# Kernel optimization log

Measured on AMD Instinct MI355X. Metric: run time of the kernel, lower is better.

## Reference

```python
import jax, jax.numpy as jnp
import numpy as np

B, S, T = 32, 512, 512           # batch, text len, decoder steps
ENC, ATT = 512, 128              # encoder_dim, attention_dim
PH, PO = 256, 256                # prenet hidden/output
DEC, M = 1024, 128               # decoder_rnn_dim, num_mels


def setup_inputs() -> dict:
    key = jax.random.key(0)
    ks = jax.random.split(key, 16)

    def w(k, shape, fan_in):
        return jax.random.normal(k, shape, jnp.float32) / np.float32(np.sqrt(fan_in))

    return {
        "encoder_outputs": jax.random.normal(ks[0], (B, S, ENC), jnp.float32),
        "target_mels": jax.random.normal(ks[1], (B, T, M), jnp.float32),
        # PreNet (dropout in eval mode => identity)
        "pn_w1": w(ks[2], (M, PH), M), "pn_b1": jnp.zeros((PH,), jnp.float32),
        "pn_w2": w(ks[3], (PH, PO), PH), "pn_b2": jnp.zeros((PO,), jnp.float32),
        # AdditiveAttention
        "att_we": w(ks[4], (ENC, ATT), ENC), "att_be": jnp.zeros((ATT,), jnp.float32),
        "att_wd": w(ks[5], (DEC, ATT), DEC), "att_bd": jnp.zeros((ATT,), jnp.float32),
        "att_v": w(ks[6], (ATT,), ATT), "att_vb": jnp.zeros((), jnp.float32),
        # GRU (PyTorch layout: W_ih [3H, in], W_hh [3H, H], gate order r,z,n)
        "gru_wih": w(ks[7], (3 * DEC, PO + ENC), PO + ENC),
        "gru_whh": w(ks[8], (3 * DEC, DEC), DEC),
        "gru_bih": jnp.zeros((3 * DEC,), jnp.float32),
        "gru_bhh": jnp.zeros((3 * DEC,), jnp.float32),
        # output / stop projections
        "out_w": w(ks[9], (DEC + ENC, M), DEC + ENC), "out_b": jnp.zeros((M,), jnp.float32),
        "stop_w": w(ks[10], (DEC + ENC, 1), DEC + ENC), "stop_b": jnp.zeros((1,), jnp.float32),
    }


def reference(encoder_outputs, target_mels, pn_w1, pn_b1, pn_w2, pn_b2,
              att_we, att_be, att_wd, att_bd, att_v, att_vb,
              gru_wih, gru_whh, gru_bih, gru_bhh,
              out_w, out_b, stop_w, stop_b):
    b, t, m = target_mels.shape
    # encoder projection is time-invariant: hoist out of the step loop
    enc_proj = encoder_outputs @ att_we + att_be              # [B,S,A]

    # teacher forcing: prev_mel at step 0 is zeros, then target_mels[:, t-1]
    prev_mels = jnp.concatenate(
        [jnp.zeros((1, b, m), target_mels.dtype),
         jnp.transpose(target_mels, (1, 0, 2))[:-1]], axis=0)  # [T,B,M]

    h0 = jnp.zeros((b, gru_whh.shape[1]), encoder_outputs.dtype)  # [B,DEC]

    def step(h, prev_mel):
        # PreNet (eval mode: dropout = identity)
        x = jax.nn.relu(prev_mel @ pn_w1 + pn_b1)
        x = jax.nn.relu(x @ pn_w2 + pn_b2)                     # [B,PO]
        # additive attention
        dproj = h @ att_wd + att_bd                            # [B,A]
        scores = jnp.tanh(enc_proj + dproj[:, None, :]) @ att_v + att_vb  # [B,S]
        aw = jax.nn.softmax(scores, axis=1)                    # [B,S]
        context = jnp.einsum('bs,bse->be', aw, encoder_outputs)  # [B,ENC]
        # GRU cell (PyTorch gate math, order r,z,n)
        rin = jnp.concatenate([x, context], axis=-1)           # [B,PO+ENC]
        gi = rin @ gru_wih.T + gru_bih                         # [B,3*DEC]
        gh = h @ gru_whh.T + gru_bhh
        ir, iz, inn = jnp.split(gi, 3, axis=-1)
        hr, hz, hn = jnp.split(gh, 3, axis=-1)
        r = jax.nn.sigmoid(ir + hr)
        z = jax.nn.sigmoid(iz + hz)
        n = jnp.tanh(inn + r * hn)
        h_new = (1.0 - z) * n + z * h                          # [B,DEC]
        # projections
        dout = jnp.concatenate([h_new, context], axis=-1)      # [B,DEC+ENC]
        mel = dout @ out_w + out_b                             # [B,M]
        stop = (dout @ stop_w + stop_b)[:, 0]                  # [B]
        return h_new, (mel, stop, aw)

    _, (mels, stops, aws) = jax.lax.scan(step, h0, prev_mels)
    mel_outputs = jnp.transpose(mels, (1, 0, 2))               # [B,T,M]
    stop_tokens = stops.T                                      # [B,T]
    attention_weights = jnp.transpose(aws, (1, 0, 2))          # [B,T,S]
    return (mel_outputs, stop_tokens, attention_weights)
```

## Files before the change

### kernel.cpp

```cpp
#include <hip/hip_runtime.h>

constexpr int B_   = 32;
constexpr int S_   = 512;
constexpr int T_   = 512;
constexpr int ENC_ = 512;
constexpr int ATT_ = 128;
constexpr int PO_  = 256;
constexpr int DEC_ = 1024;
constexpr int M_   = 128;

constexpr int MEL_OFF  = 0;
constexpr int STOP_OFF = B_*T_*M_;
constexpr int AW_OFF   = STOP_OFF + B_*T_;

typedef __attribute__((ext_vector_type(8))) short bf16x8;
typedef __attribute__((ext_vector_type(4))) float f32x4;
typedef unsigned long long ull;

__device__ __forceinline__ float frcp(float x){ return __builtin_amdgcn_rcpf(x); }
__device__ __forceinline__ float ftanh(float x){ float e = __expf(2.f*x); return 1.f - 2.f*frcp(e + 1.f); }
__device__ __forceinline__ float fsig(float x){ return frcp(1.f + __expf(-x)); }

__device__ __forceinline__ float2 upk2(unsigned u){
    return make_float2(__builtin_bit_cast(float, u << 16),
                       __builtin_bit_cast(float, u & 0xffff0000u));
}
__device__ __forceinline__ unsigned short f2b(float f){
    unsigned u = __builtin_bit_cast(unsigned, f);
    return (unsigned short)((u + 0x7fffu + ((u >> 16) & 1u)) >> 16);
}
__device__ __forceinline__ unsigned pk2(float a, float b){
    return (unsigned)f2b(a) | ((unsigned)f2b(b) << 16);
}

__device__ __forceinline__ float ald(const float* p){
    return __hip_atomic_load(p, __ATOMIC_RELAXED, __HIP_MEMORY_SCOPE_AGENT);
}
__device__ __forceinline__ ull ald64(const void* p){
    return __hip_atomic_load((const ull*)p, __ATOMIC_RELAXED, __HIP_MEMORY_SCOPE_AGENT);
}
__device__ __forceinline__ unsigned aldu(const unsigned* p){
    return __hip_atomic_load(p, __ATOMIC_RELAXED, __HIP_MEMORY_SCOPE_AGENT);
}
__device__ __forceinline__ void astf(float* p, float v){
    __hip_atomic_store(p, v, __ATOMIC_RELAXED, __HIP_MEMORY_SCOPE_AGENT);
}
union F2U { float2 f; ull u; };
__device__ __forceinline__ void ast2f(float* p, float a, float b){
    F2U x; x.f = make_float2(a, b);
    __hip_atomic_store((ull*)p, x.u, __ATOMIC_RELAXED, __HIP_MEMORY_SCOPE_AGENT);
}
__device__ __forceinline__ void astu(unsigned* p, unsigned v){
    __hip_atomic_store(p, v, __ATOMIC_RELAXED, __HIP_MEMORY_SCOPE_AGENT);
}

__device__ __forceinline__ void waitP64(const unsigned* f, unsigned ep){
    if (threadIdx.x < 64){
        for (;;){
            unsigned v = aldu(&f[threadIdx.x*16]);
            if (__all(v >= ep)) break;
            __builtin_amdgcn_s_sleep(1);
        }
    }
    __syncthreads();
}
__device__ __forceinline__ void waitP128(const unsigned* f, unsigned ep){
    if (threadIdx.x < 64){
        for (;;){
            unsigned a = aldu(&f[threadIdx.x*16]);
            unsigned b = aldu(&f[(threadIdx.x + 64)*16]);
            unsigned m = a < b ? a : b;
            if (__all(m >= ep)) break;
            __builtin_amdgcn_s_sleep(1);
        }
    }
    __syncthreads();
}
__device__ __forceinline__ void signalF(unsigned* f, unsigned v){
    asm volatile("s_waitcnt vmcnt(0) lgkmcnt(0)" ::: "memory");
    __syncthreads();
    if (threadIdx.x == 0) astu(f, v);
}

__device__ __forceinline__ f32x4 mfma16(bf16x8 a, bf16x8 b, f32x4 c){
    return __builtin_amdgcn_mfma_f32_16x16x32_bf16(a, b, c, 0, 0, 0);
}

__global__ __launch_bounds__(256) void k_prep_w(const float* __restrict__ enc,
        const float* __restrict__ whh, const float* __restrict__ wih,
        const float* __restrict__ oww,
        unsigned short* __restrict__ enc_b, unsigned short* __restrict__ wgh,
        unsigned short* __restrict__ wgx, unsigned short* __restrict__ wgc,
        unsigned short* __restrict__ ow_b){
    long long idx = (long long)blockIdx.x*256 + threadIdx.x;
    if (idx < 8388608LL){
        int bh = (int)(idx >> 17); int r = (int)(idx & 131071);
        int s = r >> 9, e = r & 511;
        int b = bh >> 1, half = bh & 1;
        enc_b[idx] = f2b(enc[((size_t)b*S_ + half*256 + s)*ENC_ + e]);
    } else if (idx < 11534336LL){
        long long q = idx - 8388608LL;
        int ds = (int)(q / 98304); int r = (int)(q % 98304);
        int jc = r / 16384; int r2 = r % 16384;
        int kc = r2 >> 9, l = (r2 >> 3) & 63, e = r2 & 7;
        int j = (jc >> 1)*1024 + ds*32 + (jc & 1)*16 + (l & 15);
        int k = kc*32 + ((l >> 4) << 3) + e;
        wgh[q] = f2b(whh[(size_t)j*DEC_ + k]);
    } else if (idx < 12320768LL){
        long long q = idx - 11534336LL;
        int ds = (int)(q / 24576); int r = (int)(q % 24576);
        int jc = r / 4096; int r3 = r % 4096;
        int kc = r3 >> 9, l = (r3 >> 3) & 63, e = r3 & 7;
        int j = (jc >> 1)*1024 + ds*32 + (jc & 1)*16 + (l & 15);
        int k = kc*32 + ((l >> 4) << 3) + e;
        wgx[q] = f2b(wih[(size_t)j*768 + k]);
    } else if (idx < 13893632LL){
        long long q = idx - 12320768LL;
        int ds = (int)(q / 49152); int r = (int)(q % 49152);
        int jc = r / 8192; int r3 = r % 8192;
        int kc = r3 >> 9, l = (r3 >> 3) & 63, e = r3 & 7;
        int j = (jc >> 1)*1024 + ds*32 + (jc & 1)*16 + (l & 15);
        int k = kc*32 + ((l >> 4) << 3) + e;
        wgc[q] = f2b(wih[(size_t)j*768 + 256 + k]);
    } else if (idx < 14090240LL){
        long long q = idx - 13893632LL;
        int cg = (int)(q / 49152); int r = (int)(q % 49152);
        int oc = r / 1536, k = r % 1536;
        ow_b[q] = f2b(oww[(size_t)k*M_ + cg*32 + oc]);
    }
}

__global__ __launch_bounds__(256) void k_encproj(const float* __restrict__ enc,
        const float* __restrict__ we, const float* __restrict__ be,
        unsigned short* __restrict__ ep_b){
    __shared__ float we_s[64*128];
    __shared__ float enc_s[64*64];
    int blk = blockIdx.x, tid = threadIdx.x;
    int b = blk >> 3, ss = blk & 7;
    int s = tid >> 2, ag = tid & 3;
    float acc[32];
    #pragma unroll
    for (int j = 0; j < 32; ++j) acc[j] = 0.f;
    for (int kc = 0; kc < 8; ++kc){
        __syncthreads();
        for (int i = tid; i < 8192; i += 256)
            we_s[i] = we[(size_t)(kc*64 + (i >> 7))*ATT_ + (i & 127)];
        for (int i = tid; i < 4096; i += 256)
            enc_s[i] = enc[((size_t)b*S_ + ss*64 + (i >> 6))*ENC_ + kc*64 + (i & 63)];
        __syncthreads();
        for (int kk = 0; kk < 64; ++kk){
            float ev = enc_s[s*64 + kk];
            const float* wr = &we_s[(kk << 7) + (ag << 5)];
            #pragma unroll
            for (int j = 0; j < 32; ++j) acc[j] += ev*wr[j];
        }
    }
    #pragma unroll
    for (int j = 0; j < 32; ++j){
        int a = (ag << 5) + j;
        ep_b[((size_t)b*512 + ss*64 + s)*ATT_ + a] = f2b(acc[j] + be[a]);
    }
}

__global__ __launch_bounds__(128) void k_prenet(const float* __restrict__ tm,
        const float* __restrict__ w1, const float* __restrict__ b1,
        const float* __restrict__ w2, const float* __restrict__ b2,
        unsigned short* __restrict__ xall){
    __shared__ float mel_l[128*20];
    __shared__ float h1_l[256*20];
    int row0 = blockIdx.x << 4;
    int t = row0 >> 5, b0 = row0 & 31;
    int tid = threadIdx.x;
    for (int p = 0; p < 16; p++){
        int idx = tid + (p << 7);
        int k = idx & 127, r = idx >> 7;
        float v = 0.f;
        if (t > 0) v = tm[((size_t)(b0 + r)*T_ + (t - 1))*M_ + k];
        mel_l[k*20 + r] = v;
    }
    __syncthreads();
    float acc1[16], acc2[16];
    #pragma unroll
    for (int i = 0; i < 16; i++){ acc1[i] = 0.f; acc2[i] = 0.f; }
    for (int k = 0; k < M_; k++){
        float wa = w1[k*256 + tid];
        float wb = w1[k*256 + tid + 128];
        float mv[16];
        *(float4*)&mv[0]  = *(const float4*)&mel_l[k*20 + 0];
        *(float4*)&mv[4]  = *(const float4*)&mel_l[k*20 + 4];
        *(float4*)&mv[8]  = *(const float4*)&mel_l[k*20 + 8];
        *(float4*)&mv[12] = *(const float4*)&mel_l[k*20 + 12];
        #pragma unroll
        for (int r = 0; r < 16; r++){ acc1[r] += mv[r]*wa; acc2[r] += mv[r]*wb; }
    }
    float bb1a = b1[tid], bb1b = b1[tid + 128];
    #pragma unroll
    for (int r = 0; r < 16; r++){
        h1_l[tid*20 + r]         = fmaxf(acc1[r] + bb1a, 0.f);
        h1_l[(tid + 128)*20 + r] = fmaxf(acc2[r] + bb1b, 0.f);
    }
    __syncthreads();
    #pragma unroll
    for (int i = 0; i < 16; i++){ acc1[i] = 0.f; acc2[i] = 0.f; }
    for (int k = 0; k < 256; k++){
        float wa = w2[k*256 + tid];
        float wb = w2[k*256 + tid + 128];
        float mv[16];
        *(float4*)&mv[0]  = *(const float4*)&h1_l[k*20 + 0];
        *(float4*)&mv[4]  = *(const float4*)&h1_l[k*20 + 4];
        *(float4*)&mv[8]  = *(const float4*)&h1_l[k*20 + 8];
        *(float4*)&mv[12] = *(const float4*)&h1_l[k*20 + 12];
        #pragma unroll
        for (int r = 0; r < 16; r++){ acc1[r] += mv[r]*wa; acc2[r] += mv[r]*wb; }
    }
    float bb2a = b2[tid], bb2b = b2[tid + 128];
    #pragma unroll
    for (int r = 0; r < 16; r++){
        xall[((size_t)row0 + r)*PO_ + tid]       = f2b(fmaxf(acc1[r] + bb2a, 0.f));
        xall[((size_t)row0 + r)*PO_ + tid + 128] = f2b(fmaxf(acc2[r] + bb2b, 0.f));
    }
}

#define DYN_BYTES 110592

struct KP {
    const unsigned short* xall_b; const unsigned short* enc_b; const unsigned short* ep_b;
    const unsigned short* wgh; const unsigned short* wgx; const unsigned short* wgc;
    const unsigned short* ow_b;
    const float* awd; const float* sw; const float* bd; const float* av; const float* avb;
    const float* bih; const float* bhh; const float* p_ob; const float* p_sb;
    float* h_f32; unsigned short* h_fb;
    unsigned short* ctx_b; float* den; float* es_b; float* dpp;
    unsigned* gflag; unsigned* aflag; unsigned* mflag; float* out;
};

__global__ __launch_bounds__(1024) void k_persist(KP p){
    extern __shared__ char sm[];
    const int bid = blockIdx.x, tid = threadIdx.x;
    const int lane = tid & 63;

    if (bid < 64){
        const int xcd = bid & 7, slot8 = bid >> 3;
        const int ds = xcd*4 + (slot8 >> 1), bh = slot8 & 1;
        unsigned short* hf_b = (unsigned short*)sm;
        char* cf = sm;
        float* pgh_l = (float*)(sm + 32768);
        float* pgx_l = (float*)(sm + 45568);
        float* pgc_l = (float*)(sm + 58368);
        float* h_l   = (float*)(sm + 71168);
        float* rden_l= (float*)(sm + 73216);
        float h_reg = 0.f;

        for (int t = 0; t < T_; ++t){
            waitP64(p.gflag, (unsigned)t);
            {
                const ull* shb = (const ull*)p.h_fb + (size_t)(t & 1)*8192;
                for (int i = tid; i < 4096; i += 1024){
                    int u = i & 1, l = (i >> 1) & 63, kc = i >> 7;
                    ((ull*)hf_b)[i] = ald64(&shb[(((size_t)bh*32 + kc)*64 + l)*2 + u]);
                }
                __syncthreads();
                int w = tid >> 6;
                if (w < 12){
                    int jc = w >> 1, kg = w & 1;
                    int r4 = lane >> 4, c16 = lane & 15;
                    const bf16x8* Bh = (const bf16x8*)p.wgh +
                        ((size_t)(ds*6 + jc)*32)*64 + lane;
                    f32x4 acc = {0.f,0.f,0.f,0.f};
                    #pragma unroll
                    for (int c = 0; c < 16; ++c){
                        int kc = kg*16 + c;
                        bf16x8 a = *(const bf16x8*)(hf_b + ((kc*64 + lane) << 3));
                        acc = mfma16(a, Bh[kc*64], acc);
                    }
                    #pragma unroll
                    for (int r = 0; r < 4; ++r)
                        pgh_l[(kg*16 + r4*4 + r)*100 + jc*16 + c16] = acc[r];
                    const bf16x8* Xp = (const bf16x8*)p.wgx +
                        ((size_t)(ds*6 + jc)*8)*64 + lane;
                    f32x4 ax = {0.f,0.f,0.f,0.f};
                    #pragma unroll
                    for (int c = 0; c < 4; ++c){
                        int kc = kg*4 + c;
                        bf16x8 a = *(const bf16x8*)(p.xall_b +
                            ((size_t)t*32 + bh*16 + c16)*256 + kc*32 + r4*8);
                        ax = mfma16(a, Xp[kc*64], ax);
                    }
                    #pragma unroll
                    for (int r = 0; r < 4; ++r)
                        pgx_l[(kg*16 + r4*4 + r)*100 + jc*16 + c16] = ax[r];
                }
                __syncthreads();
            }
            waitP64(p.aflag, (unsigned)(t + 1));
            {
                const int slot = t & 3;
                if (tid < 16){
                    int b = bh*16 + tid;
                    rden_l[tid] = frcp(ald(&p.den[slot*64 + b]) +
                                       ald(&p.den[slot*64 + 32 + b]));
                }
                __syncthreads();
                {
                    int i = tid;
                    int kc = i >> 6, l = i & 63;
                    int b = bh*16 + (l & 15);
                    int e0 = kc*32 + ((l >> 4) << 3);
                    const ull* c0 = (const ull*)p.ctx_b + (((size_t)slot*2 + 0)*32 + b)*128 + (e0 >> 2);
                    const ull* c1 = (const ull*)p.ctx_b + (((size_t)slot*2 + 1)*32 + b)*128 + (e0 >> 2);
                    ull u00 = ald64(c0), u01 = ald64(c0 + 1);
                    ull u10 = ald64(c1), u11 = ald64(c1 + 1);
                    float rd = rden_l[l & 15];
                    uint2 x0 = __builtin_bit_cast(uint2, u00);
                    uint2 x1 = __builtin_bit_cast(uint2, u01);
                    uint2 y0 = __builtin_bit_cast(uint2, u10);
                    uint2 y1 = __builtin_bit_cast(uint2, u11);
                    float2 a0 = upk2(x0.x), b0 = upk2(y0.x);
                    float2 a1 = upk2(x0.y), b1 = upk2(y0.y);
                    float2 a2 = upk2(x1.x), b2 = upk2(y1.x);
                    float2 a3 = upk2(x1.y), b3 = upk2(y1.y);
                    unsigned w0 = pk2((a0.x + b0.x)*rd, (a0.y + b0.y)*rd);
                    unsigned w1 = pk2((a1.x + b1.x)*rd, (a1.y + b1.y)*rd);
                    unsigned w2 = pk2((a2.x + b2.x)*rd, (a2.y + b2.y)*rd);
                    unsigned w3 = pk2((a3.x + b3.x)*rd, (a3.y + b3.y)*rd);
                    *(uint4*)(cf + (size_t)i*16) = make_uint4(w0, w1, w2, w3);
                }
                __syncthreads();
                int w = tid >> 6;
                if (w < 12){
                    int jc = w >> 1, kg = w & 1;
                    int r4 = lane >> 4, c16 = lane & 15;
                    const bf16x8* Cp = (const bf16x8*)p.wgc +
                        ((size_t)(ds*6 + jc)*16)*64 + lane;
                    f32x4 acc = {0.f,0.f,0.f,0.f};
                    #pragma unroll
                    for (int c = 0; c < 8; ++c){
                        int kc = kg*8 + c;
                        bf16x8 a = *(const bf16x8*)(cf + ((kc*64 + lane) << 4));
                        acc = mfma16(a, Cp[kc*64], acc);
                    }
                    #pragma unroll
                    for (int r = 0; r < 4; ++r)
                        pgc_l[(kg*16 + r4*4 + r)*100 + jc*16 + c16] = acc[r];
                }
                __syncthreads();
                if (tid < 512){
                    int b16 = tid >> 5, dl = tid & 31;
                    int dglob = ds*32 + dl;
                    const float* pa = pgh_l + b16*100;
                    const float* pb = pgh_l + (16 + b16)*100;
                    const float* xa = pgx_l + b16*100;
                    const float* xb = pgx_l + (16 + b16)*100;
                    const float* ca = pgc_l + b16*100;
                    const float* cb = pgc_l + (16 + b16)*100;
                    float gi_r = xa[dl]      + xb[dl]      + ca[dl]      + cb[dl]      + p.bih[dglob];
                    float gi_z = xa[32 + dl] + xb[32 + dl] + ca[32 + dl] + cb[32 + dl] + p.bih[1024 + dglob];
                    float gi_n = xa[64 + dl] + xb[64 + dl] + ca[64 + dl] + cb[64 + dl] + p.bih[2048 + dglob];
                    float gh_r = pa[dl]      + pb[dl]      + p.bhh[dglob];
                    float gh_z = pa[32 + dl] + pb[32 + dl] + p.bhh[1024 + dglob];
                    float gh_n = pa[64 + dl] + pb[64 + dl] + p.bhh[2048 + dglob];
                    float rr = fsig(gi_r + gh_r);
                    float zz = fsig(gi_z + gh_z);
                    float nn = ftanh(gi_n + rr*gh_n);
                    float hv = (1.f - zz)*nn + zz*h_reg;
                    h_reg = hv;
                    h_l[b16*32 + dl] = hv;
                    float hv1 = __shfl_xor(hv, 1);
                    if (!(dl & 1)){
                        int b = bh*16 + b16;
                        ast2f(&p.h_f32[(size_t)((t + 1) & 3)*32768 + (size_t)b*1024 + dglob], hv, hv1);
                        unsigned pkv = pk2(hv, hv1);
                        int l2 = ((dl >> 3) << 4) + b16;
                        size_t fo = (size_t)((t + 1) & 1)*16384 +
                                    (((size_t)bh*32 + ds)*64 + l2)*4 + ((dl & 7) >> 1);
                        astu((unsigned*)p.h_fb + fo, pkv);
                    }
                }
                __syncthreads();
                {
                    int b16 = tid >> 6, ag = tid & 63;
                    int a0 = ag*2;
                    const float* ar = p.awd + (size_t)(ds*32)*128 + a0;
                    float s0 = 0.f, s1 = 0.f;
                    #pragma unroll 8
                    for (int dl = 0; dl < 32; ++dl){
                        float hd = h_l[b16*32 + dl];
                        float2 w2 = *(const float2*)(ar + (size_t)dl*128);
                        s0 += hd*w2.x; s1 += hd*w2.y;
                    }
                    ast2f(&p.dpp[(((size_t)ds*2 + bh)*16 + b16)*128 + a0], s0, s1);
                }
            }
            signalF(&p.gflag[bid*16], (unsigned)(t + 1));
        }
    } else if (bid < 128){
        const int aa = bid - 64, b = aa >> 1, half = aa & 1;
        unsigned short* ep_l = (unsigned short*)sm;
        float* red  = (float*)(sm + 67584);
        float* sred = (float*)(sm + 100992);
        float* dpl  = (float*)(sm + 105088);
        float* avl  = (float*)(sm + 105600);
        float* esl  = (float*)(sm + 106112);
        float* eslt = (float*)(sm + 107136);
        {
            const ull* src = (const ull*)(p.ep_b + ((size_t)b*512 + half*256)*128);
            for (int i = tid; i < 8192; i += 1024){
                int row = i >> 5, col = i & 31;
                ((ull*)ep_l)[(size_t)row*33 + col] = src[i];
            }
            if (tid < 128) avl[tid] = p.av[tid];
        }
        __syncthreads();
        for (int t = 0; t < T_; ++t){
            waitP64(p.gflag, (unsigned)t);
            if (t >= 3) waitP128(p.mflag, (unsigned)(t - 2));
            const int slot = t & 3;
            {
                int a = tid & 127, g = tid >> 7;
                const int bhb = b >> 4, b15 = b & 15;
                float s = 0.f;
                #pragma unroll
                for (int i = 0; i < 4; ++i){
                    int ds2 = g*4 + i;
                    s += ald(&p.dpp[(((size_t)ds2*2 + bhb)*16 + b15)*128 + a]);
                }
                red[g*128 + a] = s;
            }
            __syncthreads();
            if (tid < 128){
                float s = p.bd[tid];
                #pragma unroll
                for (int g = 0; g < 8; ++g) s += red[g*128 + tid];
                dpl[tid] = s;
            }
            __syncthreads();
            {
                int s = tid >> 2, ao = tid & 3;
                const ull* er = (const ull*)ep_l + (size_t)s*33 + ao*8;
                float sc = 0.f;
                #pragma unroll
                for (int i = 0; i < 8; ++i){
                    uint2 uu = __builtin_bit_cast(uint2, er[i]);
                    float2 e0 = upk2(uu.x), e1 = upk2(uu.y);
                    int a0 = ao*32 + i*4;
                    sc += ftanh(e0.x + dpl[a0])*avl[a0]
                        + ftanh(e0.y + dpl[a0+1])*avl[a0+1]
                        + ftanh(e1.x + dpl[a0+2])*avl[a0+2]
                        + ftanh(e1.y + dpl[a0+3])*avl[a0+3];
                }
                sred[tid] = sc;
            }
            __syncthreads();
            if (tid < 256){
                float sc = sred[tid*4] + sred[tid*4+1] + sred[tid*4+2] + sred[tid*4+3] + p.avb[0];
                float ev = __expf(sc);
                esl[tid] = ev;
                eslt[(tid & 15)*17 + (tid >> 4)] = ev;
                astf(&p.es_b[(size_t)slot*16384 + b*512 + half*256 + tid], ev);
            }
            __syncthreads();
            if (tid < 64){
                float d = esl[tid*4] + esl[tid*4+1] + esl[tid*4+2] + esl[tid*4+3];
                #pragma unroll
                for (int m = 1; m <= 32; m <<= 1) d += __shfl_xor(d, m);
                if (tid == 0) astf(&p.den[slot*64 + half*32 + b], d);
            }
            {
                int eo = tid >> 4, sg = tid & 15;
                int e8 = eo*8;
                const unsigned short* eb = p.enc_b + ((size_t)b*2 + half)*131072;
                float a0=0,a1=0,a2=0,a3=0,a4=0,a5=0,a6=0,a7=0;
                #pragma unroll 4
                for (int i = 0; i < 16; ++i){
                    int s = sg*16 + i;
                    float ev = eslt[i*17 + sg];
                    uint4 u = *(const uint4*)(eb + (size_t)s*512 + e8);
                    float2 v0=upk2(u.x), v1=upk2(u.y), v2=upk2(u.z), v3=upk2(u.w);
                    a0+=ev*v0.x; a1+=ev*v0.y; a2+=ev*v1.x; a3+=ev*v1.y;
                    a4+=ev*v2.x; a5+=ev*v2.y; a6+=ev*v3.x; a7+=ev*v3.y;
                }
                float* rr = &red[sg*522 + e8];
                rr[0]=a0; rr[1]=a1; rr[2]=a2; rr[3]=a3;
                rr[4]=a4; rr[5]=a5; rr[6]=a6; rr[7]=a7;
            }
            __syncthreads();
            if (tid < 512){
                float c = 0.f;
                #pragma unroll
                for (int sg = 0; sg < 16; ++sg) c += red[sg*522 + tid];
                float c1 = __shfl_xor(c, 1);
                if (!(tid & 1))
                    astu((unsigned*)p.ctx_b + (((size_t)slot*2 + half)*32 + b)*256 + (tid >> 1),
                         pk2(c, c1));
            }
            signalF(&p.aflag[aa*16], (unsigned)(t + 1));
        }
    } else {
        const int m = bid - 128, b = m >> 2, q = m & 3;
        unsigned short* ow_l = (unsigned short*)sm;
        float* dout = (float*)(sm + 98432);
        float* redm = (float*)(sm + 104576);
        float* rdm  = (float*)(sm + 108800);
        float* stpr = (float*)(sm + 108816);
        {
            const ull* src = (const ull*)p.ow_b + (size_t)q*12288;
            for (int i = tid; i < 12288; i += 1024){
                int oc = i / 384, kq = i - oc*384;
                uint2 u = __builtin_bit_cast(uint2, src[i]);
                unsigned* d = (unsigned*)ow_l + (size_t)oc*769 + kq*2;
                d[0] = u.x; d[1] = u.y;
            }
        }
        __syncthreads();
        for (int t = 1; t <= T_; ++t){
            waitP64(p.gflag, (unsigned)t);
            waitP64(p.aflag, (unsigned)t);
            const int slot = (t - 1) & 3;
            if (tid < 512){
                ull u = ald64((const ull*)p.h_f32 + (size_t)(t & 3)*16384 + (size_t)b*512 + tid);
                *(float2*)&dout[tid*2] = __builtin_bit_cast(float2, u);
            } else if (tid < 768){
                int i = tid - 512;
                unsigned u0 = aldu((const unsigned*)p.ctx_b + (((size_t)slot*2 + 0)*32 + b)*256 + i);
                unsigned u1 = aldu((const unsigned*)p.ctx_b + (((size_t)slot*2 + 1)*32 + b)*256 + i);
                float2 f0 = upk2(u0), f1 = upk2(u1);
                *(float2*)&dout[1024 + i*2] = make_float2(f0.x + f1.x, f0.y + f1.y);
            } else if (tid == 1023){
                rdm[0] = frcp(ald(&p.den[slot*64 + b]) + ald(&p.den[slot*64 + 32 + b]));
            }
            __syncthreads();
            if (tid < 512) dout[1024 + tid] *= rdm[0];
            __syncthreads();
            {
                int kg = tid >> 5, oc = tid & 31;
                const unsigned* wr = (const unsigned*)ow_l + (size_t)oc*769 + kg*24;
                const float* dr = dout + kg*48;
                float a = 0.f;
                #pragma unroll 6
                for (int i = 0; i < 24; ++i){
                    float2 w2 = upk2(wr[i]);
                    a += dr[i*2]*w2.x + dr[i*2+1]*w2.y;
                }
                redm[kg*33 + oc] = a;
            }
            if (q == 0 && tid < 512){
                int k3 = tid*3;
                float s = dout[k3]*p.sw[k3] + dout[k3+1]*p.sw[k3+1] + dout[k3+2]*p.sw[k3+2];
                #pragma unroll
                for (int mm = 1; mm <= 32; mm <<= 1) s += __shfl_xor(s, mm);
                if ((tid & 63) == 0) stpr[tid >> 6] = s;
                float ev = ald(&p.es_b[(size_t)slot*16384 + b*512 + tid]);
                p.out[AW_OFF + ((size_t)b*T_ + (t-1))*S_ + tid] = ev*rdm[0];
            }
            __syncthreads();
            if (tid < 32){
                float a = 0.f;
                #pragma unroll
                for (int kg = 0; kg < 32; ++kg) a += redm[kg*33 + tid];
                int c = q*32 + tid;
                p.out[MEL_OFF + ((size_t)b*T_ + (t-1))*M_ + c] = a + p.p_ob[c];
            } else if (tid == 32 && q == 0){
                float tot = 0.f;
                #pragma unroll
                for (int w2 = 0; w2 < 8; ++w2) tot += stpr[w2];
                p.out[STOP_OFF + (size_t)b*T_ + (t-1)] = tot + p.p_sb[0];
            }
            signalF(&p.mflag[m*16], (unsigned)t);
        }
    }
}

extern "C" void kernel_launch(void* const* d_in, const int* in_sizes, int n_in,
                              void* d_out, int out_size, void* d_ws, size_t ws_size,
                              hipStream_t stream){
    const float* enc = (const float*)d_in[0];
    const float* tm  = (const float*)d_in[1];
    const float* pw1 = (const float*)d_in[2];
    const float* pb1 = (const float*)d_in[3];
    const float* pw2 = (const float*)d_in[4];
    const float* pb2 = (const float*)d_in[5];
    const float* awe = (const float*)d_in[6];
    const float* abe = (const float*)d_in[7];
    const float* awd = (const float*)d_in[8];
    const float* abd = (const float*)d_in[9];
    const float* av  = (const float*)d_in[10];
    const float* avb = (const float*)d_in[11];
    const float* wih = (const float*)d_in[12];
    const float* whh = (const float*)d_in[13];
    const float* bih = (const float*)d_in[14];
    const float* bhh = (const float*)d_in[15];
    const float* oww = (const float*)d_in[16];
    const float* obb = (const float*)d_in[17];
    const float* sww = (const float*)d_in[18];
    const float* sbb = (const float*)d_in[19];
    float* out = (float*)d_out;
    float* ws  = (float*)d_ws;

    unsigned short* xall_b = (unsigned short*)ws;
    unsigned short* enc_b  = (unsigned short*)(ws + 2097152);
    unsigned short* ep_b   = (unsigned short*)(ws + 6291456);
    unsigned short* wgh    = (unsigned short*)(ws + 7340032);
    unsigned short* wgx    = (unsigned short*)(ws + 8912896);
    unsigned short* wgc    = (unsigned short*)(ws + 9306112);
    unsigned short* ow_b   = (unsigned short*)(ws + 10092544);
    float* h_f32 = ws + 10190848;
    unsigned short* h_fb   = (unsigned short*)(ws + 10321920);
    unsigned short* ctx_b  = (unsigned short*)(ws + 10354688);
    float* den  = ws + 10420224;
    float* es_b = ws + 10420480;
    float* dpp  = ws + 10486016;
    unsigned* gflag = (unsigned*)(ws + 10617088);
    unsigned* aflag = gflag + 1024;
    unsigned* mflag = aflag + 1024;

    hipMemsetAsync(h_f32, 0, (size_t)131072*4, stream);
    hipMemsetAsync(h_fb, 0, (size_t)65536*2, stream);
    hipMemsetAsync(dpp, 0, (size_t)131072*4, stream);
    hipMemsetAsync(gflag, 0, 16384, stream);

    k_prep_w<<<55040, 256, 0, stream>>>(enc, whh, wih, oww,
                                        enc_b, wgh, wgx, wgc, ow_b);
    k_encproj<<<256, 256, 0, stream>>>(enc, awe, abe, ep_b);
    k_prenet<<<1024, 128, 0, stream>>>(tm, pw1, pb1, pw2, pb2, xall_b);

    hipFuncSetAttribute((const void*)k_persist,
                        hipFuncAttributeMaxDynamicSharedMemorySize, DYN_BYTES);

    KP kp;
    kp.xall_b = xall_b; kp.enc_b = enc_b; kp.ep_b = ep_b;
    kp.wgh = wgh; kp.wgx = wgx; kp.wgc = wgc; kp.ow_b = ow_b;
    kp.awd = awd; kp.sw = sww; kp.bd = abd; kp.av = av; kp.avb = avb;
    kp.bih = bih; kp.bhh = bhh; kp.p_ob = obb; kp.p_sb = sbb;
    kp.h_f32 = h_f32; kp.h_fb = h_fb;
    kp.ctx_b = ctx_b; kp.den = den; kp.es_b = es_b; kp.dpp = dpp;
    kp.gflag = gflag; kp.aflag = aflag; kp.mflag = mflag; kp.out = out;

    KP* kparg = &kp;
    void* args[] = { (void*)kparg };
    hipLaunchCooperativeKernel((void*)k_persist, dim3(256), dim3(1024),
                               args, DYN_BYTES, stream);
}
```

Before: 15.28 ms.

## Move decoder-state attention projection from GRU blocks into attention blocks

GRU blocks no longer compute partial h·W_d products into a global dpp buffer. Each attention block now loads the full fp32 hidden state for its batch row and computes the 128-wide projection itself against a transposed fp32 copy of att_wd made in the prep kernel. This removes a __syncthreads and a matvec from the GRU critical path and drops the dpp scratch buffer. The cost is a 1024-long dot product per attention block each step, duplicated across the two halves. Flag stride also shrinks from 16 to 4 words and the spin sleep doubles, which changes polling cache-line sharing and latency.

```diff
diff --git a/kernel.cpp b/kernel.cpp
--- a/kernel.cpp
+++ b/kernel.cpp
@@ -57,9 +57,9 @@
 __device__ __forceinline__ void waitP64(const unsigned* f, unsigned ep){
     if (threadIdx.x < 64){
         for (;;){
-            unsigned v = aldu(&f[threadIdx.x*16]);
+            unsigned v = aldu(&f[threadIdx.x*4]);
             if (__all(v >= ep)) break;
-            __builtin_amdgcn_s_sleep(1);
+            __builtin_amdgcn_s_sleep(2);
         }
     }
     __syncthreads();
@@ -67,11 +67,11 @@
 __device__ __forceinline__ void waitP128(const unsigned* f, unsigned ep){
     if (threadIdx.x < 64){
         for (;;){
-            unsigned a = aldu(&f[threadIdx.x*16]);
-            unsigned b = aldu(&f[(threadIdx.x + 64)*16]);
+            unsigned a = aldu(&f[threadIdx.x*4]);
+            unsigned b = aldu(&f[(threadIdx.x + 64)*4]);
             unsigned m = a < b ? a : b;
             if (__all(m >= ep)) break;
-            __builtin_amdgcn_s_sleep(1);
+            __builtin_amdgcn_s_sleep(2);
         }
     }
     __syncthreads();
@@ -88,10 +88,10 @@
 
 __global__ __launch_bounds__(256) void k_prep_w(const float* __restrict__ enc,
         const float* __restrict__ whh, const float* __restrict__ wih,
-        const float* __restrict__ oww,
+        const float* __restrict__ awd, const float* __restrict__ oww,
         unsigned short* __restrict__ enc_b, unsigned short* __restrict__ wgh,
         unsigned short* __restrict__ wgx, unsigned short* __restrict__ wgc,
-        unsigned short* __restrict__ ow_b){
+        unsigned short* __restrict__ ow_b, float* __restrict__ wdT32){
     long long idx = (long long)blockIdx.x*256 + threadIdx.x;
     if (idx < 8388608LL){
         int bh = (int)(idx >> 17); int r = (int)(idx & 131071);
@@ -127,6 +127,10 @@
         int cg = (int)(q / 49152); int r = (int)(q % 49152);
         int oc = r / 1536, k = r % 1536;
         ow_b[q] = f2b(oww[(size_t)k*M_ + cg*32 + oc]);
+    } else if (idx < 14221312LL){
+        long long q = idx - 14090240LL;
+        int a = (int)(q >> 10), k = (int)(q & 1023);
+        wdT32[q] = awd[(size_t)k*M_ + a];
     }
 }
 
@@ -227,10 +231,10 @@
     const unsigned short* xall_b; const unsigned short* enc_b; const unsigned short* ep_b;
     const unsigned short* wgh; const unsigned short* wgx; const unsigned short* wgc;
     const unsigned short* ow_b;
-    const float* awd; const float* sw; const float* bd; const float* av; const float* avb;
+    const float* wdT32; const float* sw; const float* bd; const float* av; const float* avb;
     const float* bih; const float* bhh; const float* p_ob; const float* p_sb;
     float* h_f32; unsigned short* h_fb;
-    unsigned short* ctx_b; float* den; float* es_b; float* dpp;
+    unsigned short* ctx_b; float* den; float* es_b;
     unsigned* gflag; unsigned* aflag; unsigned* mflag; float* out;
 };
 
@@ -247,7 +251,6 @@
         float* pgh_l = (float*)(sm + 32768);
         float* pgx_l = (float*)(sm + 45568);
         float* pgc_l = (float*)(sm + 58368);
-        float* h_l   = (float*)(sm + 71168);
         float* rden_l= (float*)(sm + 73216);
         float h_reg = 0.f;
 
@@ -364,7 +367,6 @@
                     float nn = ftanh(gi_n + rr*gh_n);
                     float hv = (1.f - zz)*nn + zz*h_reg;
                     h_reg = hv;
-                    h_l[b16*32 + dl] = hv;
                     float hv1 = __shfl_xor(hv, 1);
                     if (!(dl & 1)){
                         int b = bh*16 + b16;
@@ -376,28 +378,15 @@
                         astu((unsigned*)p.h_fb + fo, pkv);
                     }
                 }
-                __syncthreads();
-                {
-                    int b16 = tid >> 6, ag = tid & 63;
-                    int a0 = ag*2;
-                    const float* ar = p.awd + (size_t)(ds*32)*128 + a0;
-                    float s0 = 0.f, s1 = 0.f;
-                    #pragma unroll 8
-                    for (int dl = 0; dl < 32; ++dl){
-                        float hd = h_l[b16*32 + dl];
-                        float2 w2 = *(const float2*)(ar + (size_t)dl*128);
-                        s0 += hd*w2.x; s1 += hd*w2.y;
-                    }
-                    ast2f(&p.dpp[(((size_t)ds*2 + bh)*16 + b16)*128 + a0], s0, s1);
-                }
-            }
-            signalF(&p.gflag[bid*16], (unsigned)(t + 1));
+            }
+            signalF(&p.gflag[bid*4], (unsigned)(t + 1));
         }
     } else if (bid < 128){
         const int aa = bid - 64, b = aa >> 1, half = aa & 1;
         unsigned short* ep_l = (unsigned short*)sm;
         float* red  = (float*)(sm + 67584);
         float* sred = (float*)(sm + 100992);
+        float* h_lf = (float*)(sm + 100992);
         float* dpl  = (float*)(sm + 105088);
         float* avl  = (float*)(sm + 105600);
         float* esl  = (float*)(sm + 106112);
@@ -415,16 +404,22 @@
             waitP64(p.gflag, (unsigned)t);
             if (t >= 3) waitP128(p.mflag, (unsigned)(t - 2));
             const int slot = t & 3;
+            if (tid < 512)
+                ((ull*)h_lf)[tid] = ald64((const ull*)p.h_f32 +
+                    (size_t)(t & 3)*16384 + (size_t)b*512 + tid);
+            __syncthreads();
             {
-                int a = tid & 127, g = tid >> 7;
-                const int bhb = b >> 4, b15 = b & 15;
+                int a = tid & 127, kg = tid >> 7;
+                const float* hw = h_lf + kg*128;
+                const float* wr = p.wdT32 + (size_t)a*1024 + kg*128;
                 float s = 0.f;
-                #pragma unroll
-                for (int i = 0; i < 4; ++i){
-                    int ds2 = g*4 + i;
-                    s += ald(&p.dpp[(((size_t)ds2*2 + bhb)*16 + b15)*128 + a]);
-                }
-                red[g*128 + a] = s;
+                #pragma unroll 8
+                for (int i = 0; i < 128; i += 4){
+                    float4 h4 = *(const float4*)(hw + i);
+                    float4 w4 = *(const float4*)(wr + i);
+                    s += h4.x*w4.x + h4.y*w4.y + h4.z*w4.z + h4.w*w4.w;
+                }
+                red[kg*128 + a] = s;
             }
             __syncthreads();
             if (tid < 128){
@@ -493,7 +488,7 @@
                     astu((unsigned*)p.ctx_b + (((size_t)slot*2 + half)*32 + b)*256 + (tid >> 1),
                          pk2(c, c1));
             }
-            signalF(&p.aflag[aa*16], (unsigned)(t + 1));
+            signalF(&p.aflag[aa*4], (unsigned)(t + 1));
         }
     } else {
         const int m = bid - 128, b = m >> 2, q = m & 3;
@@ -565,7 +560,7 @@
                 for (int w2 = 0; w2 < 8; ++w2) tot += stpr[w2];
                 p.out[STOP_OFF + (size_t)b*T_ + (t-1)] = tot + p.p_sb[0];
             }
-            signalF(&p.mflag[m*16], (unsigned)t);
+            signalF(&p.mflag[m*4], (unsigned)t);
         }
     }
 }
@@ -608,18 +603,17 @@
     unsigned short* ctx_b  = (unsigned short*)(ws + 10354688);
     float* den  = ws + 10420224;
     float* es_b = ws + 10420480;
-    float* dpp  = ws + 10486016;
+    float* wdT32 = ws + 10486016;
     unsigned* gflag = (unsigned*)(ws + 10617088);
-    unsigned* aflag = gflag + 1024;
-    unsigned* mflag = aflag + 1024;
+    unsigned* aflag = gflag + 256;
+    unsigned* mflag = aflag + 256;
 
     hipMemsetAsync(h_f32, 0, (size_t)131072*4, stream);
     hipMemsetAsync(h_fb, 0, (size_t)65536*2, stream);
-    hipMemsetAsync(dpp, 0, (size_t)131072*4, stream);
-    hipMemsetAsync(gflag, 0, 16384, stream);
-
-    k_prep_w<<<55040, 256, 0, stream>>>(enc, whh, wih, oww,
-                                        enc_b, wgh, wgx, wgc, ow_b);
+    hipMemsetAsync(gflag, 0, 4096, stream);
+
+    k_prep_w<<<55552, 256, 0, stream>>>(enc, whh, wih, awd, oww,
+                                        enc_b, wgh, wgx, wgc, ow_b, wdT32);
     k_encproj<<<256, 256, 0, stream>>>(enc, awe, abe, ep_b);
     k_prenet<<<1024, 128, 0, stream>>>(tm, pw1, pb1, pw2, pb2, xall_b);
 
@@ -629,10 +623,10 @@
     KP kp;
     kp.xall_b = xall_b; kp.enc_b = enc_b; kp.ep_b = ep_b;
     kp.wgh = wgh; kp.wgx = wgx; kp.wgc = wgc; kp.ow_b = ow_b;
-    kp.awd = awd; kp.sw = sww; kp.bd = abd; kp.av = av; kp.avb = avb;
+    kp.wdT32 = wdT32; kp.sw = sww; kp.bd = abd; kp.av = av; kp.avb = avb;
     kp.bih = bih; kp.bhh = bhh; kp.p_ob = obb; kp.p_sb = sbb;
     kp.h_f32 = h_f32; kp.h_fb = h_fb;
-    kp.ctx_b = ctx_b; kp.den = den; kp.es_b = es_b; kp.dpp = dpp;
+    kp.ctx_b = ctx_b; kp.den = den; kp.es_b = es_b;
     kp.gflag = gflag; kp.aflag = aflag; kp.mflag = mflag; kp.out = out;
 
     KP* kparg = &kp;
```

Measured after the change: 18.92 ms. +23.8%, slower.
